# Kernel optimization log

Hardware: AMD Instinct MI355X
Metric: run time of the kernel (lower is better)

## Reference

```python
import jax, jax.numpy as jnp
import numpy as np

B, S, D, H, DFF = 2, 4096, 256, 8, 1024
DK = D // H


def setup_inputs() -> dict:
    key = jax.random.key(0)
    ks = jax.random.split(key, 12)
    sc = 0.02
    inp = {
        "x": jax.random.normal(ks[0], (B, S, D), jnp.float32),
        "mask": jnp.ones((B, 1, 1, S), jnp.int32),
        "Wq": jax.random.normal(ks[1], (D, D), jnp.float32) * sc,
        "bq": jnp.zeros((D,), jnp.float32),
        "Wk": jax.random.normal(ks[2], (D, D), jnp.float32) * sc,
        "bk": jnp.zeros((D,), jnp.float32),
        "Wv": jax.random.normal(ks[3], (D, D), jnp.float32) * sc,
        "bv": jnp.zeros((D,), jnp.float32),
        "Wo": jax.random.normal(ks[4], (D, D), jnp.float32) * sc,
        "bo": jnp.zeros((D,), jnp.float32),
        "W1": jax.random.normal(ks[5], (D, DFF), jnp.float32) * sc,
        "b1": jnp.zeros((DFF,), jnp.float32),
        "W2": jax.random.normal(ks[6], (DFF, D), jnp.float32) * sc,
        "b2": jnp.zeros((D,), jnp.float32),
        "g1": jnp.ones((D,), jnp.float32),
        "be1": jnp.zeros((D,), jnp.float32),
        "g2": jnp.ones((D,), jnp.float32),
        "be2": jnp.zeros((D,), jnp.float32),
        "a1": jnp.float32(1e-8),
        "a2": jnp.float32(1e-8),
    }
    return inp


def _layernorm(x, g, b, eps=1e-5):
    mu = jnp.mean(x, axis=-1, keepdims=True)
    var = jnp.var(x, axis=-1, keepdims=True)
    return (x - mu) * jax.lax.rsqrt(var + eps) * g + b


def _block(x, mask, Wq, bq, Wk, bk, Wv, bv, Wo, bo, W1, b1, W2, b2, g1, be1, g2, be2, a1, a2):
    # multi-head attention (dropout = identity in eval)
    def proj(W, b):
        return (x @ W + b).reshape(B, S, H, DK).transpose(0, 2, 1, 3)  # [B,H,S,DK]
    q, k, v = proj(Wq, bq), proj(Wk, bk), proj(Wv, bv)
    scores = jnp.einsum("bhsd,bhtd->bhst", q, k) / jnp.sqrt(jnp.float32(DK))
    scores = jnp.where(mask == 0, jnp.float32(-1e9), scores)
    p_attn = jax.nn.softmax(scores, axis=-1)
    ctx = jnp.einsum("bhst,bhtd->bhsd", p_attn, v)
    ctx = ctx.transpose(0, 2, 1, 3).reshape(B, S, D)
    attn_out = ctx @ Wo + bo
    x1 = _layernorm(x + a1 * attn_out, g1, be1)
    # FFN
    h = jax.nn.gelu(x1 @ W1 + b1, approximate=False)
    ffn_out = h @ W2 + b2
    return _layernorm(x1 + a2 * ffn_out, g2, be2)


def reference(x, mask, Wq, bq, Wk, bk, Wv, bv, Wo, bo, W1, b1, W2, b2, g1, be1, g2, be2, a1, a2):
    return _block(x, mask, Wq, bq, Wk, bk, Wv, bv, Wo, bo, W1, b1, W2, b2, g1, be1, g2, be2, a1, a2)
```

## Files before the change

kernel.cpp:

```cpp
#include <hip/hip_runtime.h>
#include <hip/hip_bf16.h>
#include <math.h>

#define B_ 2
#define S_ 4096
#define D_ 256
#define H_ 8
#define DFF_ 1024
#define DK_ 32

typedef __attribute__((ext_vector_type(8))) short short8;
typedef __attribute__((ext_vector_type(4))) float f32x4;
typedef __attribute__((ext_vector_type(16))) float f32x16;
typedef __attribute__((ext_vector_type(4))) int int4v;

__device__ __forceinline__ unsigned short f2bf(float f) {
  unsigned int u = __builtin_bit_cast(unsigned int, f);
  u += 0x7FFFu + ((u >> 16) & 1u);
  return (unsigned short)(u >> 16);
}

__device__ __forceinline__ float bf2f(unsigned short s) {
  unsigned int u = ((unsigned int)s) << 16;
  return __builtin_bit_cast(float, u);
}

__device__ __forceinline__ short8 u32x4_to_s8(unsigned int a, unsigned int b,
                                              unsigned int c, unsigned int d) {
  int4v v = {(int)a, (int)b, (int)c, (int)d};
  return __builtin_bit_cast(short8, v);
}

__global__ __launch_bounds__(256) void k_prepw(
    const float* __restrict__ Wq, const float* __restrict__ Wk,
    const float* __restrict__ Wv, const float* __restrict__ Wo,
    const float* __restrict__ W1, const float* __restrict__ W2,
    const float* __restrict__ bq, const float* __restrict__ bk,
    const float* __restrict__ bv, const float* __restrict__ x,
    unsigned short* __restrict__ WqkvT, unsigned short* __restrict__ WoT,
    unsigned short* __restrict__ W1T, unsigned short* __restrict__ W2T,
    float* __restrict__ bqkv, unsigned short* __restrict__ xb) {
  const float k2 = 0.25500525551f;
  int bx = blockIdx.x, t = threadIdx.x;
  if (bx < 768) {
    int which = bx >> 8;
    int i = ((bx & 255) << 8) | t;
    const float* W = (which == 0) ? Wq : (which == 1) ? Wk : Wv;
    int n = i >> 8, k = i & 255;
    float v = W[k * 256 + n] * ((which == 0) ? k2 : 1.0f);
    WqkvT[(size_t)(which * 256 + n) * 256 + k] = f2bf(v);
  } else if (bx < 1024) {
    int i = ((bx - 768) << 8) | t;
    int n = i >> 8, k = i & 255;
    WoT[i] = f2bf(Wo[k * 256 + n]);
  } else if (bx < 2048) {
    int i = ((bx - 1024) << 8) | t;
    int n = i >> 8, k = i & 255;
    W1T[i] = f2bf(W1[k * 1024 + n]);
  } else if (bx < 3072) {
    int i = ((bx - 2048) << 8) | t;
    int n = i >> 10, k = i & 1023;
    W2T[i] = f2bf(W2[k * 256 + n]);
  } else if (bx < 3075) {
    int i = ((bx - 3072) << 8) | t;
    if (i < 768) bqkv[i] = (i < 256) ? bq[i] * k2 : (i < 512) ? bk[i - 256] : bv[i - 512];
  } else {
    int i = (bx - 3075) * 2048 + t * 8;
    f32x4 f0 = *(const f32x4*)(x + i);
    f32x4 f1 = *(const f32x4*)(x + i + 4);
    short8 o;
#pragma unroll
    for (int e = 0; e < 4; e++) { o[e] = (short)f2bf(f0[e]); o[e + 4] = (short)f2bf(f1[e]); }
    *(short8*)(xb + i) = o;
  }
}

__global__ __launch_bounds__(256) void k_gemmqkv(const unsigned short* __restrict__ A,
                                                 const unsigned short* __restrict__ Bt,
                                                 const float* __restrict__ bias,
                                                 unsigned short* __restrict__ qb,
                                                 unsigned short* __restrict__ kpk,
                                                 unsigned short* __restrict__ vpk) {
  const int K = 256;
  __shared__ unsigned short Al[128][40];
  __shared__ unsigned short Bl[64][40];
  const int tid = threadIdx.x;
  const int wid = tid >> 6, lane = tid & 63;
  const int lhi = lane >> 4, llo = lane & 15;
  const int rowbase = wid * 32;
  const int bm = blockIdx.x, bn = blockIdx.y;

  f32x4 zero = {0.f, 0.f, 0.f, 0.f};
  f32x4 acc[2][4];
#pragma unroll
  for (int m = 0; m < 2; m++)
#pragma unroll
    for (int n = 0; n < 4; n++) acc[m][n] = zero;

  const int r0 = tid >> 2, c8 = (tid & 3) * 8;
  const unsigned short* A16a = A + (size_t)(bm * 128 + r0) * K + c8;
  const unsigned short* A16b = A + (size_t)(bm * 128 + r0 + 64) * K + c8;
  const unsigned short* Brow0 = Bt + (size_t)(bn * 64 + r0) * K + c8;

  for (int kb = 0; kb < K; kb += 32) {
    __syncthreads();
    *(short8*)&Al[r0][c8] = *(const short8*)(A16a + kb);
    *(short8*)&Al[r0 + 64][c8] = *(const short8*)(A16b + kb);
    *(short8*)&Bl[r0][c8] = *(const short8*)(Brow0 + kb);
    __syncthreads();
    short8 af[2], bf[4];
#pragma unroll
    for (int m = 0; m < 2; m++) af[m] = *(const short8*)&Al[rowbase + m * 16 + llo][lhi * 8];
#pragma unroll
    for (int n = 0; n < 4; n++) bf[n] = *(const short8*)&Bl[n * 16 + llo][lhi * 8];
#pragma unroll
    for (int m = 0; m < 2; m++)
#pragma unroll
      for (int n = 0; n < 4; n++)
        acc[m][n] = __builtin_amdgcn_mfma_f32_16x16x32_bf16(af[m], bf[n], acc[m][n], 0, 0, 0);
  }

  const int which = bn >> 2;
#pragma unroll
  for (int m = 0; m < 2; m++)
#pragma unroll
    for (int n = 0; n < 4; n++)
#pragma unroll
      for (int r = 0; r < 4; r++) {
        int row = bm * 128 + rowbase + m * 16 + lhi * 4 + r;
        int gcol = bn * 64 + n * 16 + llo;
        int col0 = gcol - which * 256;
        float v = acc[m][n][r] + bias[gcol];
        unsigned short bv = f2bf(v);
        int t = row & (S_ - 1), b = row >> 12;
        int h = col0 >> 5;
        if (which == 0) {
          qb[(size_t)row * 256 + col0] = bv;
        } else if (which == 1) {
          int c5 = col0 & 31, jj = (c5 >> 4) & 1, hik = (c5 >> 3) & 1, e = c5 & 7;
          int tile = t >> 6, i = (t >> 5) & 1, l31k = t & 31;
          size_t addr = (((size_t)(b * 8 + h) * 64 + tile) * 4 + i * 2 + jj) * 512 +
                        (hik * 32 + l31k) * 8 + e;
          kpk[addr] = bv;
        } else {
          int d = col0 & 31;
          int x5 = t >> 6, j = (t >> 3) & 7, kk = t & 7;
          size_t addr = (((size_t)(b * 8 + h) * 64 + x5) * 4 + (j >> 1)) * 512 +
                        ((j & 1) * 32 + d) * 8 + kk;
          vpk[addr] = bv;
        }
      }
}

__global__ __launch_bounds__(256) void k_gemm1(const unsigned short* __restrict__ A,
                                               const unsigned short* __restrict__ Bt,
                                               const float* __restrict__ bias,
                                               unsigned short* __restrict__ Cout,
                                               int M, int N, int K) {
  __shared__ unsigned short Al[128][40];
  __shared__ unsigned short Bl[128][40];
  const int tid = threadIdx.x;
  const int wid = tid >> 6, lane = tid & 63;
  const int lhi = lane >> 4, llo = lane & 15;
  const int wr = wid >> 1, wc = wid & 1;
  const int rowbase = wr * 64, colbase = wc * 64;
  const int bm = blockIdx.x, bn = blockIdx.y;

  f32x4 zero = {0.f, 0.f, 0.f, 0.f};
  f32x4 acc[4][4];
#pragma unroll
  for (int m = 0; m < 4; m++)
#pragma unroll
    for (int n = 0; n < 4; n++) acc[m][n] = zero;

  const int r0 = tid >> 2, c8 = (tid & 3) * 8;
  const unsigned short* A16a = A + (size_t)(bm * 128 + r0) * K + c8;
  const unsigned short* A16b = A + (size_t)(bm * 128 + r0 + 64) * K + c8;
  const unsigned short* Brow0 = Bt + (size_t)(bn * 128 + r0) * K + c8;
  const unsigned short* Brow1 = Bt + (size_t)(bn * 128 + r0 + 64) * K + c8;

  for (int kb = 0; kb < K; kb += 32) {
    __syncthreads();
    *(short8*)&Al[r0][c8] = *(const short8*)(A16a + kb);
    *(short8*)&Al[r0 + 64][c8] = *(const short8*)(A16b + kb);
    *(short8*)&Bl[r0][c8] = *(const short8*)(Brow0 + kb);
    *(short8*)&Bl[r0 + 64][c8] = *(const short8*)(Brow1 + kb);
    __syncthreads();
    short8 af[4], bf[4];
#pragma unroll
    for (int m = 0; m < 4; m++) af[m] = *(const short8*)&Al[rowbase + m * 16 + llo][lhi * 8];
#pragma unroll
    for (int n = 0; n < 4; n++) bf[n] = *(const short8*)&Bl[colbase + n * 16 + llo][lhi * 8];
#pragma unroll
    for (int m = 0; m < 4; m++)
#pragma unroll
      for (int n = 0; n < 4; n++)
        acc[m][n] = __builtin_amdgcn_mfma_f32_16x16x32_bf16(af[m], bf[n], acc[m][n], 0, 0, 0);
  }

#pragma unroll
  for (int m = 0; m < 4; m++)
#pragma unroll
    for (int n = 0; n < 4; n++)
#pragma unroll
      for (int r = 0; r < 4; r++) {
        int row = bm * 128 + rowbase + m * 16 + lhi * 4 + r;
        int col = bn * 128 + colbase + n * 16 + llo;
        float v = acc[m][n][r] + bias[col];
        v = 0.5f * v * (1.0f + erff(v * 0.70710678118f));
        Cout[(size_t)row * N + col] = f2bf(v);
      }
}

template <int BASE16, int OUT32>
__global__ __launch_bounds__(512) void k_gemmln(const unsigned short* __restrict__ A,
                                                const unsigned short* __restrict__ Bt,
                                                const float* __restrict__ bias,
                                                const void* __restrict__ base,
                                                const float* __restrict__ alpha,
                                                const float* __restrict__ g,
                                                const float* __restrict__ be,
                                                void* __restrict__ y, int K) {
  __shared__ unsigned short Al[2][32][40];
  __shared__ unsigned short Bl[2][256][40];
  __shared__ float psum[32][4], psq[32][4];
  float* partial = (float*)&Bl[0][0][0];

  const int tid = threadIdx.x;
  const int w = tid >> 6, lane = tid & 63;
  const int kh = w >> 2, wc = w & 3;
  const int lhi = lane >> 4, llo = lane & 15;
  const int row0 = blockIdx.x * 32;
  const int Kh = K >> 1;

  f32x4 zero = {0.f, 0.f, 0.f, 0.f};
  f32x4 acc[2][4];
#pragma unroll
  for (int m = 0; m < 2; m++)
#pragma unroll
    for (int n = 0; n < 4; n++) acc[m][n] = zero;

  for (int kb = 0; kb < Kh; kb += 32) {
    __syncthreads();
    if (tid < 256) {
      int kh2 = tid >> 7, ra = (tid >> 2) & 31, ca = (tid & 3) * 8;
      *(short8*)&Al[kh2][ra][ca] =
          *(const short8*)(A + (size_t)(row0 + ra) * K + kh2 * Kh + kb + ca);
    }
#pragma unroll
    for (int s = 0; s < 4; s++) {
      int c = tid + s * 512;
      int kh2 = c >> 10, rb = (c >> 2) & 255, cb = (c & 3) * 8;
      *(short8*)&Bl[kh2][rb][cb] =
          *(const short8*)(Bt + (size_t)rb * K + kh2 * Kh + kb + cb);
    }
    __syncthreads();
    short8 af[2], bf[4];
#pragma unroll
    for (int m = 0; m < 2; m++) af[m] = *(const short8*)&Al[kh][m * 16 + llo][lhi * 8];
#pragma unroll
    for (int n = 0; n < 4; n++)
      bf[n] = *(const short8*)&Bl[kh][wc * 64 + n * 16 + llo][lhi * 8];
#pragma unroll
    for (int m = 0; m < 2; m++)
#pragma unroll
      for (int n = 0; n < 4; n++)
        acc[m][n] = __builtin_amdgcn_mfma_f32_16x16x32_bf16(af[m], bf[n], acc[m][n], 0, 0, 0);
  }

  __syncthreads();
  if (kh == 1) {
#pragma unroll
    for (int m = 0; m < 2; m++)
#pragma unroll
      for (int n = 0; n < 4; n++)
#pragma unroll
        for (int r = 0; r < 4; r++) {
          int lrow = m * 16 + lhi * 4 + r;
          int col = wc * 64 + n * 16 + llo;
          partial[lrow * 256 + col] = acc[m][n][r];
        }
  }
  __syncthreads();

  const float a = alpha[0];
  const unsigned short* b16 = (const unsigned short*)base;
  const float* b32 = (const float*)base;

  if (kh == 0) {
#pragma unroll
    for (int m = 0; m < 2; m++)
#pragma unroll
      for (int r = 0; r < 4; r++) {
        int lrow = m * 16 + lhi * 4 + r;
        size_t grow = (size_t)(row0 + lrow);
        float s = 0.f, q = 0.f;
#pragma unroll
        for (int n = 0; n < 4; n++) {
          int col = wc * 64 + n * 16 + llo;
          float v = acc[m][n][r] + partial[lrow * 256 + col] + bias[col];
          float xb = BASE16 ? bf2f(b16[grow * 256 + col]) : b32[grow * 256 + col];
          float rr = fmaf(a, v, xb);
          acc[m][n][r] = rr;
          s += rr;
          q = fmaf(rr, rr, q);
        }
#pragma unroll
        for (int off = 1; off < 16; off <<= 1) {
          s += __shfl_xor(s, off);
          q += __shfl_xor(q, off);
        }
        if (llo == 0) { psum[lrow][wc] = s; psq[lrow][wc] = q; }
      }
  }
  __syncthreads();

  if (kh == 0) {
#pragma unroll
    for (int m = 0; m < 2; m++)
#pragma unroll
      for (int r = 0; r < 4; r++) {
        int lrow = m * 16 + lhi * 4 + r;
        size_t grow = (size_t)(row0 + lrow);
        float S = psum[lrow][0] + psum[lrow][1] + psum[lrow][2] + psum[lrow][3];
        float Q = psq[lrow][0] + psq[lrow][1] + psq[lrow][2] + psq[lrow][3];
        float mu = S * (1.0f / 256.0f);
        float var = Q * (1.0f / 256.0f) - mu * mu;
        float rs = rsqrtf(var + 1e-5f);
#pragma unroll
        for (int n = 0; n < 4; n++) {
          int col = wc * 64 + n * 16 + llo;
          float o = (acc[m][n][r] - mu) * rs * g[col] + be[col];
          if (OUT32) ((float*)y)[grow * 256 + col] = o;
          else ((unsigned short*)y)[grow * 256 + col] = f2bf(o);
        }
      }
  }
}

__global__ __launch_bounds__(512, 2) void k_attn(const unsigned short* __restrict__ qb,
                                                 const unsigned short* __restrict__ kpk,
                                                 const unsigned short* __restrict__ vpk,
                                                 const int* __restrict__ mask,
                                                 unsigned short* __restrict__ ctx) {
  __shared__ float accS[4][32][32];
  __shared__ float lS[4][32];
  const int tid = threadIdx.x;
  const int lane = tid & 63;
  const int w = tid >> 6;
  const int qt = w >> 1, half = w & 1;
  const int l31 = lane & 31, hi = lane >> 5;
  const int q0 = blockIdx.x * 128 + qt * 32;
  const int h = blockIdx.y, b = blockIdx.z;
  const size_t bS = (size_t)b * S_;

  const unsigned short* Qp = qb + (bS + q0 + l31) * 256 + h * DK_ + hi * 8;
  short8 qf0 = *(const short8*)Qp;
  short8 qf1 = *(const short8*)(Qp + 16);

  const size_t fragbase = ((size_t)(b * H_ + h) * 64 + half * 32) * 2048 + lane * 8;
  const unsigned short* kp = kpk + fragbase;
  const unsigned short* vp = vpk + fragbase;
  const int* mp = mask + bS + half * 2048 + lane;

  f32x16 acc, lacc;
#pragma unroll
  for (int r = 0; r < 16; r++) { acc[r] = 0.f; lacc[r] = 0.f; }
  const f32x16 zz = acc;
  short8 ones;
#pragma unroll
  for (int e = 0; e < 8; e++) ones[e] = (short)0x3F80;

  short8 kf0, kf1, kf2, kf3, vf0, vf1, vf2, vf3;
  unsigned int pk0[8], pk1[8];
  f32x16 s0, s1;

#define LDKF() { kf0 = *(const short8*)(kp); kf1 = *(const short8*)(kp + 512); \
                 kf2 = *(const short8*)(kp + 1024); kf3 = *(const short8*)(kp + 1536); kp += 2048; }
#define LDVF() { vf0 = *(const short8*)(vp); vf1 = *(const short8*)(vp + 512); \
                 vf2 = *(const short8*)(vp + 1024); vf3 = *(const short8*)(vp + 1536); vp += 2048; }
#define QKM() {                                                                  \
    s0 = __builtin_amdgcn_mfma_f32_32x32x16_bf16(kf0, qf0, zz, 0, 0, 0);         \
    s1 = __builtin_amdgcn_mfma_f32_32x32x16_bf16(kf2, qf0, zz, 0, 0, 0);         \
    s0 = __builtin_amdgcn_mfma_f32_32x32x16_bf16(kf1, qf1, s0, 0, 0, 0);         \
    s1 = __builtin_amdgcn_mfma_f32_32x32x16_bf16(kf3, qf1, s1, 0, 0, 0);         \
  }
#define EXPM(mv) {                                                               \
    unsigned long long bal = __ballot((mv) != 0);                                \
    if (__builtin_expect(bal != ~0ull, 0)) {                                     \
      _Pragma("unroll") for (int r = 0; r < 16; r++) {                           \
        int tt = (r & 3) + 8 * (r >> 2) + 4 * hi;                                \
        if (!((bal >> tt) & 1)) s0[r] = -3e38f;                                  \
        if (!((bal >> (tt + 32)) & 1)) s1[r] = -3e38f;                           \
      }                                                                          \
    }                                                                            \
    _Pragma("unroll") for (int r = 0; r < 16; r++) {                             \
      s0[r] = __builtin_amdgcn_exp2f(s0[r]);                                     \
      s1[r] = __builtin_amdgcn_exp2f(s1[r]);                                     \
    }                                                                            \
    _Pragma("unroll") for (int j = 0; j < 8; j++) {                              \
      asm("v_cvt_pk_bf16_f32 %0, %1, %2" : "=v"(pk0[j]) : "v"(s0[2*j]), "v"(s0[2*j+1])); \
      asm("v_cvt_pk_bf16_f32 %0, %1, %2" : "=v"(pk1[j]) : "v"(s1[2*j]), "v"(s1[2*j+1])); \
    }                                                                            \
  }
#define PVM() {                                                                  \
    __builtin_amdgcn_s_setprio(1);                                               \
    _Pragma("unroll") for (int kk = 0; kk < 4; kk++) {                           \
      unsigned int* pk = (kk < 2) ? pk0 : pk1;                                   \
      int base = (kk & 1) * 4;                                                   \
      auto r02 = __builtin_amdgcn_permlane32_swap(pk[base], pk[base + 2], false, false);     \
      auto r13 = __builtin_amdgcn_permlane32_swap(pk[base + 1], pk[base + 3], false, false); \
      short8 pfr = u32x4_to_s8(r02[0], r13[0], r02[1], r13[1]);                  \
      short8 vv = (kk == 0) ? vf0 : (kk == 1) ? vf1 : (kk == 2) ? vf2 : vf3;     \
      acc = __builtin_amdgcn_mfma_f32_32x32x16_bf16(pfr, vv, acc, 0, 0, 0);      \
      lacc = __builtin_amdgcn_mfma_f32_32x32x16_bf16(pfr, ones, lacc, 0, 0, 0);  \
    }                                                                            \
    __builtin_amdgcn_s_setprio(0);                                               \
  }

  LDKF();
  int mvC = mp[0];
  int mvN = mp[64];
  QKM();
  LDKF();
  LDVF();
  EXPM(mvC);
  mvC = mvN;
  mvN = mp[128];

  for (int t = 1; t < 32; ++t) {
    QKM();
    LDKF();
    PVM();
    LDVF();
    EXPM(mvC);
    mvC = mvN;
    mvN = mp[(t + 2 < 32 ? t + 2 : 31) * 64];
  }
  PVM();

  if (half == 1) {
#pragma unroll
    for (int r = 0; r < 16; r++) {
      int q = (r & 3) + 8 * (r >> 2) + 4 * hi;
      accS[qt][q][l31] = acc[r];
    }
    if (l31 == 0) {
#pragma unroll
      for (int r = 0; r < 16; r++) {
        int q = (r & 3) + 8 * (r >> 2) + 4 * hi;
        lS[qt][q] = lacc[r];
      }
    }
  }
  __syncthreads();
  if (half == 0) {
#pragma unroll
    for (int r = 0; r < 16; r++) {
      int q = (r & 3) + 8 * (r >> 2) + 4 * hi;
      float o = acc[r] + accS[qt][q][l31];
      float L = lacc[r] + lS[qt][q];
      ctx[(bS + q0 + q) * (size_t)D_ + h * DK_ + l31] = f2bf(o / L);
    }
  }
#undef LDKF
#undef LDVF
#undef QKM
#undef EXPM
#undef PVM
}

extern "C" void kernel_launch(void* const* d_in, const int* in_sizes, int n_in,
                              void* d_out, int out_size, void* d_ws, size_t ws_size,
                              hipStream_t stream) {
  const float* x   = (const float*)d_in[0];
  const int* mask  = (const int*)d_in[1];
  const float* Wq  = (const float*)d_in[2];
  const float* bq  = (const float*)d_in[3];
  const float* Wk  = (const float*)d_in[4];
  const float* bk  = (const float*)d_in[5];
  const float* Wv  = (const float*)d_in[6];
  const float* bv  = (const float*)d_in[7];
  const float* Wo  = (const float*)d_in[8];
  const float* bo  = (const float*)d_in[9];
  const float* W1  = (const float*)d_in[10];
  const float* b1  = (const float*)d_in[11];
  const float* W2  = (const float*)d_in[12];
  const float* b2  = (const float*)d_in[13];
  const float* g1  = (const float*)d_in[14];
  const float* be1 = (const float*)d_in[15];
  const float* g2  = (const float*)d_in[16];
  const float* be2 = (const float*)d_in[17];
  const float* a1  = (const float*)d_in[18];
  const float* a2  = (const float*)d_in[19];
  float* out = (float*)d_out;

  char* ws = (char*)d_ws;
  const size_t MB = 1024 * 1024;
  unsigned short* qb  = (unsigned short*)(ws + 0);
  unsigned short* kpk = (unsigned short*)(ws + 5 * MB);
  unsigned short* vpk = (unsigned short*)(ws + 10 * MB);
  unsigned short* ctx = (unsigned short*)(ws + 15 * MB);
  unsigned short* x1b = (unsigned short*)(ws + 19 * MB);
  unsigned short* hb  = (unsigned short*)(ws + 23 * MB);
  unsigned short* WqkvT = (unsigned short*)(ws + 40 * MB);
  unsigned short* WoT   = (unsigned short*)(ws + 40 * MB + 512 * 1024);
  unsigned short* W1T   = (unsigned short*)(ws + 41 * MB);
  unsigned short* W2T   = (unsigned short*)(ws + 41 * MB + 512 * 1024);
  float* bqkv           = (float*)(ws + 42 * MB);
  unsigned short* xb    = (unsigned short*)(ws + 43 * MB);

  const int NTOK = B_ * S_;

  k_prepw<<<dim3(4099), 256, 0, stream>>>(Wq, Wk, Wv, Wo, W1, W2, bq, bk, bv, x,
                                          WqkvT, WoT, W1T, W2T, bqkv, xb);

  k_gemmqkv<<<dim3(64, 12), 256, 0, stream>>>(xb, WqkvT, bqkv, qb, kpk, vpk);

  k_attn<<<dim3(S_ / 128, H_, B_), 512, 0, stream>>>(qb, kpk, vpk, mask, ctx);

  k_gemmln<0, 0><<<dim3(NTOK / 32), 512, 0, stream>>>(ctx, WoT, bo, x, a1, g1, be1,
                                                      x1b, 256);

  k_gemm1<<<dim3(64, 8), 256, 0, stream>>>(x1b, W1T, b1, hb, NTOK, 1024, 256);

  k_gemmln<1, 1><<<dim3(NTOK / 32), 512, 0, stream>>>(hb, W2T, b2, x1b, a2, g2, be2,
                                                      out, 1024);
}
```

Baseline: 130.9 us.

## Reuse each K/V tile across two query tiles with 4-way key split per block

The attention kernel now has each wave process two 32-row query tiles against its K/V slice, so every loaded K/V fragment feeds two QK and PV MFMA sets. The key dimension is split four ways across the waves of a 64-query block, and partial outputs and row sums are reduced through shared memory at the end. Block size drops to 256 threads with a grid twice as large. The intent is to halve K/V global loads per unit of compute. In exchange it raises register pressure from the doubled accumulators and adds a larger shared-memory reduction, which may lower occupancy.

```diff
diff --git a/kernel.cpp b/kernel.cpp
--- a/kernel.cpp
+++ b/kernel.cpp
@@ -338,35 +338,37 @@
   }
 }
 
-__global__ __launch_bounds__(512, 2) void k_attn(const unsigned short* __restrict__ qb,
+__global__ __launch_bounds__(256, 3) void k_attn(const unsigned short* __restrict__ qbuf,
                                                  const unsigned short* __restrict__ kpk,
                                                  const unsigned short* __restrict__ vpk,
                                                  const int* __restrict__ mask,
                                                  unsigned short* __restrict__ ctx) {
-  __shared__ float accS[4][32][32];
-  __shared__ float lS[4][32];
+  __shared__ float accS[4][64][32];
+  __shared__ float lS[4][64];
   const int tid = threadIdx.x;
   const int lane = tid & 63;
   const int w = tid >> 6;
-  const int qt = w >> 1, half = w & 1;
   const int l31 = lane & 31, hi = lane >> 5;
-  const int q0 = blockIdx.x * 128 + qt * 32;
+  const int q0 = blockIdx.x * 64;
   const int h = blockIdx.y, b = blockIdx.z;
   const size_t bS = (size_t)b * S_;
 
-  const unsigned short* Qp = qb + (bS + q0 + l31) * 256 + h * DK_ + hi * 8;
-  short8 qf0 = *(const short8*)Qp;
-  short8 qf1 = *(const short8*)(Qp + 16);
-
-  const size_t fragbase = ((size_t)(b * H_ + h) * 64 + half * 32) * 2048 + lane * 8;
+  const unsigned short* QpA = qbuf + (bS + q0 + l31) * 256 + h * DK_ + hi * 8;
+  short8 qa0 = *(const short8*)QpA;
+  short8 qa1 = *(const short8*)(QpA + 16);
+  const unsigned short* QpB = QpA + 32 * 256;
+  short8 qb0 = *(const short8*)QpB;
+  short8 qb1 = *(const short8*)(QpB + 16);
+
+  const size_t fragbase = ((size_t)(b * H_ + h) * 64 + w * 16) * 2048 + lane * 8;
   const unsigned short* kp = kpk + fragbase;
   const unsigned short* vp = vpk + fragbase;
-  const int* mp = mask + bS + half * 2048 + lane;
-
-  f32x16 acc, lacc;
-#pragma unroll
-  for (int r = 0; r < 16; r++) { acc[r] = 0.f; lacc[r] = 0.f; }
-  const f32x16 zz = acc;
+  const int* mp = mask + bS + w * 1024 + lane;
+
+  f32x16 accA, accB, laccA, laccB;
+#pragma unroll
+  for (int r = 0; r < 16; r++) { accA[r] = 0.f; accB[r] = 0.f; laccA[r] = 0.f; laccB[r] = 0.f; }
+  const f32x16 zz = accA;
   short8 ones;
 #pragma unroll
   for (int e = 0; e < 8; e++) ones[e] = (short)0x3F80;
@@ -379,19 +381,18 @@
                  kf2 = *(const short8*)(kp + 1024); kf3 = *(const short8*)(kp + 1536); kp += 2048; }
 #define LDVF() { vf0 = *(const short8*)(vp); vf1 = *(const short8*)(vp + 512); \
                  vf2 = *(const short8*)(vp + 1024); vf3 = *(const short8*)(vp + 1536); vp += 2048; }
-#define QKM() {                                                                  \
-    s0 = __builtin_amdgcn_mfma_f32_32x32x16_bf16(kf0, qf0, zz, 0, 0, 0);         \
-    s1 = __builtin_amdgcn_mfma_f32_32x32x16_bf16(kf2, qf0, zz, 0, 0, 0);         \
-    s0 = __builtin_amdgcn_mfma_f32_32x32x16_bf16(kf1, qf1, s0, 0, 0, 0);         \
-    s1 = __builtin_amdgcn_mfma_f32_32x32x16_bf16(kf3, qf1, s1, 0, 0, 0);         \
-  }
-#define EXPM(mv) {                                                               \
-    unsigned long long bal = __ballot((mv) != 0);                                \
-    if (__builtin_expect(bal != ~0ull, 0)) {                                     \
+#define QKM(qx0, qx1) {                                                          \
+    s0 = __builtin_amdgcn_mfma_f32_32x32x16_bf16(kf0, qx0, zz, 0, 0, 0);         \
+    s1 = __builtin_amdgcn_mfma_f32_32x32x16_bf16(kf2, qx0, zz, 0, 0, 0);         \
+    s0 = __builtin_amdgcn_mfma_f32_32x32x16_bf16(kf1, qx1, s0, 0, 0, 0);         \
+    s1 = __builtin_amdgcn_mfma_f32_32x32x16_bf16(kf3, qx1, s1, 0, 0, 0);         \
+  }
+#define EXPM(bal) {                                                              \
+    if (__builtin_expect((bal) != ~0ull, 0)) {                                   \
       _Pragma("unroll") for (int r = 0; r < 16; r++) {                           \
         int tt = (r & 3) + 8 * (r >> 2) + 4 * hi;                                \
-        if (!((bal >> tt) & 1)) s0[r] = -3e38f;                                  \
-        if (!((bal >> (tt + 32)) & 1)) s1[r] = -3e38f;                           \
+        if (!(((bal) >> tt) & 1)) s0[r] = -3e38f;                                \
+        if (!(((bal) >> (tt + 32)) & 1)) s1[r] = -3e38f;                         \
       }                                                                          \
     }                                                                            \
     _Pragma("unroll") for (int r = 0; r < 16; r++) {                             \
@@ -403,7 +404,7 @@
       asm("v_cvt_pk_bf16_f32 %0, %1, %2" : "=v"(pk1[j]) : "v"(s1[2*j]), "v"(s1[2*j+1])); \
     }                                                                            \
   }
-#define PVM() {                                                                  \
+#define PVM(accX, laccX) {                                                       \
     __builtin_amdgcn_s_setprio(1);                                               \
     _Pragma("unroll") for (int kk = 0; kk < 4; kk++) {                           \
       unsigned int* pk = (kk < 2) ? pk0 : pk1;                                   \
@@ -412,56 +413,53 @@
       auto r13 = __builtin_amdgcn_permlane32_swap(pk[base + 1], pk[base + 3], false, false); \
       short8 pfr = u32x4_to_s8(r02[0], r13[0], r02[1], r13[1]);                  \
       short8 vv = (kk == 0) ? vf0 : (kk == 1) ? vf1 : (kk == 2) ? vf2 : vf3;     \
-      acc = __builtin_amdgcn_mfma_f32_32x32x16_bf16(pfr, vv, acc, 0, 0, 0);      \
-      lacc = __builtin_amdgcn_mfma_f32_32x32x16_bf16(pfr, ones, lacc, 0, 0, 0);  \
+      accX = __builtin_amdgcn_mfma_f32_32x32x16_bf16(pfr, vv, accX, 0, 0, 0);    \
+      laccX = __builtin_amdgcn_mfma_f32_32x32x16_bf16(pfr, ones, laccX, 0, 0, 0);\
     }                                                                            \
     __builtin_amdgcn_s_setprio(0);                                               \
   }
 
   LDKF();
+  LDVF();
   int mvC = mp[0];
   int mvN = mp[64];
-  QKM();
-  LDKF();
-  LDVF();
-  EXPM(mvC);
-  mvC = mvN;
-  mvN = mp[128];
-
-  for (int t = 1; t < 32; ++t) {
-    QKM();
+
+  for (int t = 0; t < 16; ++t) {
+    unsigned long long bal = __ballot(mvC != 0);
+    QKM(qa0, qa1);
+    EXPM(bal);
+    PVM(accA, laccA);
+    QKM(qb0, qb1);
     LDKF();
-    PVM();
+    EXPM(bal);
+    PVM(accB, laccB);
     LDVF();
-    EXPM(mvC);
     mvC = mvN;
-    mvN = mp[(t + 2 < 32 ? t + 2 : 31) * 64];
-  }
-  PVM();
-
-  if (half == 1) {
+    mvN = mp[(t + 2 < 16 ? t + 2 : 15) * 64];
+  }
+
+#pragma unroll
+  for (int r = 0; r < 16; r++) {
+    int q = (r & 3) + 8 * (r >> 2) + 4 * hi;
+    accS[w][q][l31] = accA[r];
+    accS[w][q + 32][l31] = accB[r];
+  }
+  if (l31 == 0) {
 #pragma unroll
     for (int r = 0; r < 16; r++) {
       int q = (r & 3) + 8 * (r >> 2) + 4 * hi;
-      accS[qt][q][l31] = acc[r];
+      lS[w][q] = laccA[r];
+      lS[w][q + 32] = laccB[r];
     }
-    if (l31 == 0) {
-#pragma unroll
-      for (int r = 0; r < 16; r++) {
-        int q = (r & 3) + 8 * (r >> 2) + 4 * hi;
-        lS[qt][q] = lacc[r];
-      }
-    }
   }
   __syncthreads();
-  if (half == 0) {
-#pragma unroll
-    for (int r = 0; r < 16; r++) {
-      int q = (r & 3) + 8 * (r >> 2) + 4 * hi;
-      float o = acc[r] + accS[qt][q][l31];
-      float L = lacc[r] + lS[qt][q];
-      ctx[(bS + q0 + q) * (size_t)D_ + h * DK_ + l31] = f2bf(o / L);
-    }
+#pragma unroll
+  for (int i = 0; i < 8; i++) {
+    int e = tid + 256 * i;
+    int q = e >> 5, d = e & 31;
+    float o = accS[0][q][d] + accS[1][q][d] + accS[2][q][d] + accS[3][q][d];
+    float L = lS[0][q] + lS[1][q] + lS[2][q] + lS[3][q];
+    ctx[(bS + q0 + q) * (size_t)D_ + h * DK_ + d] = f2bf(o / L);
   }
 #undef LDKF
 #undef LDVF
@@ -517,7 +515,7 @@
 
   k_gemmqkv<<<dim3(64, 12), 256, 0, stream>>>(xb, WqkvT, bqkv, qb, kpk, vpk);
 
-  k_attn<<<dim3(S_ / 128, H_, B_), 512, 0, stream>>>(qb, kpk, vpk, mask, ctx);
+  k_attn<<<dim3(S_ / 64, H_, B_), 256, 0, stream>>>(qb, kpk, vpk, mask, ctx);
 
   k_gemmln<0, 0><<<dim3(NTOK / 32), 512, 0, stream>>>(ctx, WoT, bo, x, a1, g1, be1,
                                                       x1b, 256);
```

New measurement: 129.5 us. No clear change (-1.1%).
